# Optimization experiments

Hardware: AMD Instinct MI355X
Metric: run time of the kernel (lower is better)

Reference implementation:

```python
import jax, jax.numpy as jnp
import numpy as np

K_NEIGHBOURS = 2


def setup_inputs() -> dict:
    key = jax.random.key(0)
    k1, k2 = jax.random.split(key)
    train_features = jax.random.normal(k1, (200000, 128), dtype=jnp.float32)
    test_features = jax.random.normal(k2, (2048, 128), dtype=jnp.float32)
    return {"train_features": train_features, "test_features": test_features}


def reference(train_features, test_features):
    # faiss IndexFlatL2 returns SQUARED L2 distances.
    # d2[m, n] = ||q_m||^2 + ||t_n||^2 - 2 q_m . t_n
    q_sq = jnp.sum(test_features * test_features, axis=1, keepdims=True)   # [M, 1]
    t_sq = jnp.sum(train_features * train_features, axis=1)                # [N]
    cross = jnp.einsum('md,nd->mn', test_features, train_features)        # [M, N]
    d2 = q_sq + t_sq[None, :] - 2.0 * cross                               # [M, N]
    # top-2 smallest distances per query -> negate and take top_k
    neg_topk, _ = jax.lax.top_k(-d2, K_NEIGHBOURS)                        # [M, 2]
    # sum of the 2 nearest-neighbour squared distances
    return jnp.sum(-neg_topk, axis=1)                                     # [M]
```

## Files before the change

### kernel.cpp

```cpp
#include <hip/hip_runtime.h>
#include <hip/hip_bf16.h>


typedef short bf16x8 __attribute__((ext_vector_type(8)));
typedef float f32x4 __attribute__((ext_vector_type(4)));

#define N_TRAIN 200000
#define M_QUERY 2048
#define DIMS 128
#define NCHUNK 125
#define PTS_PER_CHUNK 1600
#define TB 32
#define ITERS (PTS_PER_CHUNK / TB)

__device__ __forceinline__ unsigned int bf_bits(float f) {
  unsigned int u = __float_as_uint(f);
  return (u + 0x7FFFu + ((u >> 16) & 1u)) >> 16;
}

__global__ __launch_bounds__(256) void convert_kernel(
    const float* __restrict__ src, unsigned short* __restrict__ dst,
    float* __restrict__ sq, int nrows) {
  int gtid = blockIdx.x * 256 + threadIdx.x;
  int row = gtid >> 3, sub = gtid & 7;
  if (row >= nrows) return;
  const float4* s4 = reinterpret_cast<const float4*>(src + (size_t)row * DIMS + sub * 16);
  unsigned int pk[8];
  float acc = 0.f;
#pragma unroll
  for (int i = 0; i < 4; ++i) {
    float4 v = s4[i];
    acc += v.x * v.x + v.y * v.y + v.z * v.z + v.w * v.w;
    pk[i * 2 + 0] = bf_bits(v.x) | (bf_bits(v.y) << 16);
    pk[i * 2 + 1] = bf_bits(v.z) | (bf_bits(v.w) << 16);
  }
  uint4* d4 = reinterpret_cast<uint4*>(dst + (size_t)row * DIMS + sub * 16);
  d4[0] = make_uint4(pk[0], pk[1], pk[2], pk[3]);
  d4[1] = make_uint4(pk[4], pk[5], pk[6], pk[7]);
  acc += __shfl_xor(acc, 1);
  acc += __shfl_xor(acc, 2);
  acc += __shfl_xor(acc, 4);
  if (sub == 0) sq[row] = acc;
}

__global__ __launch_bounds__(256) void knn_main(
    const unsigned short* __restrict__ tb, const unsigned short* __restrict__ qb16,
    const float* __restrict__ tsq, float* __restrict__ partials) {
  const int chunk = blockIdx.x;
  const int qblock = blockIdx.y * 256;
  const int tid = threadIdx.x;
  const int w = tid >> 6, l = tid & 63;
  const int lo = l & 15, hi = l >> 4;
  const int qw = qblock + w * 64;

  __shared__ uint4 smem4[2][512];
  char* smem = reinterpret_cast<char*>(smem4);

  bf16x8 a[4][4];
#pragma unroll
  for (int t = 0; t < 4; ++t)
#pragma unroll
    for (int kf = 0; kf < 4; ++kf)
      a[t][kf] = *reinterpret_cast<const bf16x8*>(
          qb16 + (size_t)(qw + t * 16 + lo) * DIMS + kf * 32 + hi * 8);

  const int srow = tid >> 4, sblk = tid & 15;
  const int wo = srow * 256 + (((sblk ^ (srow & 7)) << 4));
  const char* gsrc = reinterpret_cast<const char*>(tb) +
                     (size_t)chunk * PTS_PER_CHUNK * 256 + tid * 16;

  int roff[4];
#pragma unroll
  for (int kf = 0; kf < 4; ++kf)
    roff[kf] = lo * 256 + ((((kf << 2) + hi) ^ (lo & 7)) << 4);

  const float* tsp = tsq + chunk * PTS_PER_CHUNK + lo;

  const float INF = __builtin_inff();
  float best1[4][4], best2[4][4];
#pragma unroll
  for (int t = 0; t < 4; ++t)
#pragma unroll
    for (int r = 0; r < 4; ++r) { best1[t][r] = INF; best2[t][r] = INF; }

  {
    uint4 r0 = *reinterpret_cast<const uint4*>(gsrc);
    uint4 r1 = *reinterpret_cast<const uint4*>(gsrc + 4096);
    *reinterpret_cast<uint4*>(smem + wo) = r0;
    *reinterpret_cast<uint4*>(smem + wo + 4096) = r1;
    gsrc += TB * 256;
  }
  __syncthreads();

  const f32x4 z = {0.f, 0.f, 0.f, 0.f};
  int cur = 0;
  for (int it = 0; it < ITERS; ++it) {
    const bool pf = (it + 1 < ITERS);
    uint4 r0, r1;
    if (pf) {
      r0 = *reinterpret_cast<const uint4*>(gsrc);
      r1 = *reinterpret_cast<const uint4*>(gsrc + 4096);
      gsrc += TB * 256;
    }
    float tv0 = tsp[0];
    float tv1 = tsp[16];
    tsp += TB;

    const char* buf = smem + cur * 8192;
    bf16x8 f0[4], f1[4];
#pragma unroll
    for (int kf = 0; kf < 4; ++kf) {
      f0[kf] = *reinterpret_cast<const bf16x8*>(buf + roff[kf]);
      f1[kf] = *reinterpret_cast<const bf16x8*>(buf + roff[kf] + 4096);
    }

#pragma unroll
    for (int t = 0; t < 4; ++t) {
      f32x4 acc0 = __builtin_amdgcn_mfma_f32_16x16x32_bf16(a[t][0], f0[0], z, 0, 0, 0);
      f32x4 acc1 = __builtin_amdgcn_mfma_f32_16x16x32_bf16(a[t][0], f1[0], z, 0, 0, 0);
#pragma unroll
      for (int kf = 1; kf < 4; ++kf) {
        acc0 = __builtin_amdgcn_mfma_f32_16x16x32_bf16(a[t][kf], f0[kf], acc0, 0, 0, 0);
        acc1 = __builtin_amdgcn_mfma_f32_16x16x32_bf16(a[t][kf], f1[kf], acc1, 0, 0, 0);
      }
#pragma unroll
      for (int r = 0; r < 4; ++r) {
        float s0 = fmaf(-2.f, acc0[r], tv0);
        float n1 = fminf(best1[t][r], s0);
        float n2 = __builtin_amdgcn_fmed3f(best1[t][r], best2[t][r], s0);
        best1[t][r] = n1; best2[t][r] = n2;
        float s1 = fmaf(-2.f, acc1[r], tv1);
        n1 = fminf(best1[t][r], s1);
        n2 = __builtin_amdgcn_fmed3f(best1[t][r], best2[t][r], s1);
        best1[t][r] = n1; best2[t][r] = n2;
      }
    }

    if (pf) {
      char* nb = smem + (cur ^ 1) * 8192;
      *reinterpret_cast<uint4*>(nb + wo) = r0;
      *reinterpret_cast<uint4*>(nb + wo + 4096) = r1;
    }
    __syncthreads();
    cur ^= 1;
  }

#pragma unroll
  for (int t = 0; t < 4; ++t)
#pragma unroll
    for (int r = 0; r < 4; ++r) {
      float v1 = best1[t][r], v2 = best2[t][r];
#pragma unroll
      for (int m = 1; m < 16; m <<= 1) {
        float o1 = __shfl_xor(v1, m);
        float o2 = __shfl_xor(v2, m);
        float n1 = fminf(v1, o1);
        float n2 = fminf(fmaxf(v1, o1), fminf(v2, o2));
        v1 = n1;
        v2 = n2;
      }
      best1[t][r] = v1;
      best2[t][r] = v2;
    }
  if (lo == 0) {
#pragma unroll
    for (int t = 0; t < 4; ++t)
#pragma unroll
      for (int r = 0; r < 4; ++r) {
        int q = qw + t * 16 + hi * 4 + r;
        float* p = partials + ((size_t)chunk * M_QUERY + q) * 2;
        p[0] = best1[t][r];
        p[1] = best2[t][r];
      }
  }
}

__global__ __launch_bounds__(256) void knn_reduce(
    const float* __restrict__ partials, const float* __restrict__ qsq,
    float* __restrict__ out) {
  int q = blockIdx.x * 256 + threadIdx.x;
  if (q >= M_QUERY) return;
  const float INF = __builtin_inff();
  float b1 = INF, b2 = INF;
  for (int c = 0; c < NCHUNK; ++c) {
    const float* p = partials + ((size_t)c * M_QUERY + q) * 2;
    float v = p[0];
    float n1 = fminf(b1, v);
    float n2 = __builtin_amdgcn_fmed3f(b1, b2, v);
    b1 = n1; b2 = n2;
    v = p[1];
    n1 = fminf(b1, v);
    n2 = __builtin_amdgcn_fmed3f(b1, b2, v);
    b1 = n1; b2 = n2;
  }
  out[q] = 2.f * qsq[q] + b1 + b2;
}

extern "C" void kernel_launch(void* const* d_in, const int* in_sizes, int n_in,
                              void* d_out, int out_size, void* d_ws, size_t ws_size,
                              hipStream_t stream) {
  const float* train = (const float*)d_in[0];
  const float* test  = (const float*)d_in[1];
  float* out = (float*)d_out;
  char* ws = (char*)d_ws;

  size_t off_tb  = 0;
  size_t off_qb  = off_tb  + (size_t)N_TRAIN * DIMS * 2;
  size_t off_tsq = off_qb  + (size_t)M_QUERY * DIMS * 2;
  size_t off_qsq = off_tsq + (size_t)N_TRAIN * 4;
  size_t off_pt  = off_qsq + (size_t)M_QUERY * 4;
  size_t total   = off_pt  + (size_t)NCHUNK * M_QUERY * 2 * 4;
  if (ws_size < total) return;

  unsigned short* tbp = (unsigned short*)(ws + off_tb);
  unsigned short* qb  = (unsigned short*)(ws + off_qb);
  float* tsq = (float*)(ws + off_tsq);
  float* qsq = (float*)(ws + off_qsq);
  float* part = (float*)(ws + off_pt);

  hipLaunchKernelGGL(convert_kernel, dim3((N_TRAIN * 8) / 256), dim3(256), 0, stream,
                     train, tbp, tsq, N_TRAIN);
  hipLaunchKernelGGL(convert_kernel, dim3((M_QUERY * 8) / 256), dim3(256), 0, stream,
                     test, qb, qsq, M_QUERY);
  hipLaunchKernelGGL(knn_main, dim3(NCHUNK, M_QUERY / 256), dim3(256), 0, stream,
                     tbp, qb, tsq, part);
  hipLaunchKernelGGL(knn_reduce, dim3(M_QUERY / 256), dim3(256), 0, stream,
                     part, qsq, out);
}
```

Before: 170.0 us.

## Use direct global-to-LDS loads, stage tsq in LDS, and split train into more chunks

Replaces the register-staged prefetch (global load to VGPR, then LDS store) with global_load_lds direct-to-LDS transfers. The swizzle now moves to the global source address, with each wave writing its own 1KB slice. Per-chunk train norms are preloaded into shared memory, the grid is reordered so query blocks are adjacent, and launch bounds ask for 5 blocks per CU. When the workspace allows it, the train set is split into 250 chunks of 800 points, doubling block count at the cost of more partials in the reduce.

```diff
diff --git a/kernel.cpp b/kernel.cpp
--- a/kernel.cpp
+++ b/kernel.cpp
@@ -8,10 +8,7 @@
 #define N_TRAIN 200000
 #define M_QUERY 2048
 #define DIMS 128
-#define NCHUNK 125
-#define PTS_PER_CHUNK 1600
 #define TB 32
-#define ITERS (PTS_PER_CHUNK / TB)
 
 __device__ __forceinline__ unsigned int bf_bits(float f) {
   unsigned int u = __float_as_uint(f);
@@ -43,18 +40,20 @@
   if (sub == 0) sq[row] = acc;
 }
 
-__global__ __launch_bounds__(256) void knn_main(
+template <int PPC>
+__global__ __launch_bounds__(256, 5) void knn_main(
     const unsigned short* __restrict__ tb, const unsigned short* __restrict__ qb16,
     const float* __restrict__ tsq, float* __restrict__ partials) {
-  const int chunk = blockIdx.x;
-  const int qblock = blockIdx.y * 256;
+  constexpr int ITERS = PPC / TB;
+  const int chunk = blockIdx.y;
+  const int qblock = blockIdx.x * 256;
   const int tid = threadIdx.x;
   const int w = tid >> 6, l = tid & 63;
   const int lo = l & 15, hi = l >> 4;
   const int qw = qblock + w * 64;
 
-  __shared__ uint4 smem4[2][512];
-  char* smem = reinterpret_cast<char*>(smem4);
+  __shared__ char smem[2 * 8192];
+  __shared__ float tsq_s[PPC];
 
   bf16x8 a[4][4];
 #pragma unroll
@@ -65,17 +64,15 @@
           qb16 + (size_t)(qw + t * 16 + lo) * DIMS + kf * 32 + hi * 8);
 
   const int srow = tid >> 4, sblk = tid & 15;
-  const int wo = srow * 256 + (((sblk ^ (srow & 7)) << 4));
   const char* gsrc = reinterpret_cast<const char*>(tb) +
-                     (size_t)chunk * PTS_PER_CHUNK * 256 + tid * 16;
+                     (size_t)chunk * PPC * 256 + srow * 256 + ((sblk ^ (srow & 7)) << 4);
+  char* lbase = smem + w * 1024;
 
   int roff[4];
 #pragma unroll
   for (int kf = 0; kf < 4; ++kf)
     roff[kf] = lo * 256 + ((((kf << 2) + hi) ^ (lo & 7)) << 4);
 
-  const float* tsp = tsq + chunk * PTS_PER_CHUNK + lo;
-
   const float INF = __builtin_inff();
   float best1[4][4], best2[4][4];
 #pragma unroll
@@ -83,30 +80,32 @@
 #pragma unroll
     for (int r = 0; r < 4; ++r) { best1[t][r] = INF; best2[t][r] = INF; }
 
-  {
-    uint4 r0 = *reinterpret_cast<const uint4*>(gsrc);
-    uint4 r1 = *reinterpret_cast<const uint4*>(gsrc + 4096);
-    *reinterpret_cast<uint4*>(smem + wo) = r0;
-    *reinterpret_cast<uint4*>(smem + wo + 4096) = r1;
-    gsrc += TB * 256;
-  }
+  __builtin_amdgcn_global_load_lds(
+      (const __attribute__((address_space(1))) void*)gsrc,
+      (__attribute__((address_space(3))) void*)lbase, 16, 0, 0);
+  __builtin_amdgcn_global_load_lds(
+      (const __attribute__((address_space(1))) void*)(gsrc + 4096),
+      (__attribute__((address_space(3))) void*)(lbase + 4096), 16, 0, 0);
+  gsrc += TB * 256;
+  for (int i = tid; i < PPC; i += 256) tsq_s[i] = tsq[chunk * PPC + i];
   __syncthreads();
 
-  const f32x4 z = {0.f, 0.f, 0.f, 0.f};
   int cur = 0;
   for (int it = 0; it < ITERS; ++it) {
-    const bool pf = (it + 1 < ITERS);
-    uint4 r0, r1;
-    if (pf) {
-      r0 = *reinterpret_cast<const uint4*>(gsrc);
-      r1 = *reinterpret_cast<const uint4*>(gsrc + 4096);
+    if (it + 1 < ITERS) {
+      char* nb = lbase + ((cur ^ 1) << 13);
+      __builtin_amdgcn_global_load_lds(
+          (const __attribute__((address_space(1))) void*)gsrc,
+          (__attribute__((address_space(3))) void*)nb, 16, 0, 0);
+      __builtin_amdgcn_global_load_lds(
+          (const __attribute__((address_space(1))) void*)(gsrc + 4096),
+          (__attribute__((address_space(3))) void*)(nb + 4096), 16, 0, 0);
       gsrc += TB * 256;
     }
-    float tv0 = tsp[0];
-    float tv1 = tsp[16];
-    tsp += TB;
-
-    const char* buf = smem + cur * 8192;
+    float tv0 = tsq_s[it * TB + lo];
+    float tv1 = tsq_s[it * TB + 16 + lo];
+
+    const char* buf = smem + (cur << 13);
     bf16x8 f0[4], f1[4];
 #pragma unroll
     for (int kf = 0; kf < 4; ++kf) {
@@ -114,6 +113,7 @@
       f1[kf] = *reinterpret_cast<const bf16x8*>(buf + roff[kf] + 4096);
     }
 
+    const f32x4 z = {0.f, 0.f, 0.f, 0.f};
 #pragma unroll
     for (int t = 0; t < 4; ++t) {
       f32x4 acc0 = __builtin_amdgcn_mfma_f32_16x16x32_bf16(a[t][0], f0[0], z, 0, 0, 0);
@@ -135,12 +135,6 @@
         best1[t][r] = n1; best2[t][r] = n2;
       }
     }
-
-    if (pf) {
-      char* nb = smem + (cur ^ 1) * 8192;
-      *reinterpret_cast<uint4*>(nb + wo) = r0;
-      *reinterpret_cast<uint4*>(nb + wo + 4096) = r1;
-    }
     __syncthreads();
     cur ^= 1;
   }
@@ -177,12 +171,12 @@
 
 __global__ __launch_bounds__(256) void knn_reduce(
     const float* __restrict__ partials, const float* __restrict__ qsq,
-    float* __restrict__ out) {
+    float* __restrict__ out, int nchunk) {
   int q = blockIdx.x * 256 + threadIdx.x;
   if (q >= M_QUERY) return;
   const float INF = __builtin_inff();
   float b1 = INF, b2 = INF;
-  for (int c = 0; c < NCHUNK; ++c) {
+  for (int c = 0; c < nchunk; ++c) {
     const float* p = partials + ((size_t)c * M_QUERY + q) * 2;
     float v = p[0];
     float n1 = fminf(b1, v);
@@ -209,8 +203,10 @@
   size_t off_tsq = off_qb  + (size_t)M_QUERY * DIMS * 2;
   size_t off_qsq = off_tsq + (size_t)N_TRAIN * 4;
   size_t off_pt  = off_qsq + (size_t)M_QUERY * 4;
-  size_t total   = off_pt  + (size_t)NCHUNK * M_QUERY * 2 * 4;
-  if (ws_size < total) return;
+  size_t need250 = off_pt + (size_t)250 * M_QUERY * 2 * 4;
+  size_t need125 = off_pt + (size_t)125 * M_QUERY * 2 * 4;
+  if (ws_size < need125) return;
+  const bool use250 = (ws_size >= need250);
 
   unsigned short* tbp = (unsigned short*)(ws + off_tb);
   unsigned short* qb  = (unsigned short*)(ws + off_qb);
@@ -222,8 +218,15 @@
                      train, tbp, tsq, N_TRAIN);
   hipLaunchKernelGGL(convert_kernel, dim3((M_QUERY * 8) / 256), dim3(256), 0, stream,
                      test, qb, qsq, M_QUERY);
-  hipLaunchKernelGGL(knn_main, dim3(NCHUNK, M_QUERY / 256), dim3(256), 0, stream,
-                     tbp, qb, tsq, part);
-  hipLaunchKernelGGL(knn_reduce, dim3(M_QUERY / 256), dim3(256), 0, stream,
-                     part, qsq, out);
-}
+  if (use250) {
+    hipLaunchKernelGGL(knn_main<800>, dim3(8, 250), dim3(256), 0, stream,
+                       tbp, qb, tsq, part);
+    hipLaunchKernelGGL(knn_reduce, dim3(M_QUERY / 256), dim3(256), 0, stream,
+                       part, qsq, out, 250);
+  } else {
+    hipLaunchKernelGGL(knn_main<1600>, dim3(8, 125), dim3(256), 0, stream,
+                       tbp, qb, tsq, part);
+    hipLaunchKernelGGL(knn_reduce, dim3(M_QUERY / 256), dim3(256), 0, stream,
+                       part, qsq, out, 125);
+  }
+}
```

Measured after the change: 604.6 us. +255.6%, slower.
